# Performance work log

Measured on AMD Instinct MI355X. Metric: run time of the kernel, lower is better.

The kernel has to match this reference:

```python
import jax, jax.numpy as jnp
import numpy as np

E_PHI = 1024
E_F = 1024
HID = 1024
N_HEADS = 16
HEAD_DIM = HID // N_HEADS


def setup_inputs() -> dict:
    key = jax.random.key(0)
    ks = jax.random.split(key, 9)
    B, S = 2, 2048
    s = 0.02
    return {
        "q": jax.random.normal(ks[0], (B, S, E_PHI), jnp.float32),
        "k": jax.random.normal(ks[1], (B, S, E_PHI), jnp.float32),
        "v": jax.random.normal(ks[2], (B, S, E_F), jnp.float32),
        "W_q": jax.random.normal(ks[3], (E_PHI, HID), jnp.float32) * s,
        "W_k": jax.random.normal(ks[4], (E_PHI, HID), jnp.float32) * s,
        "W_v": jax.random.normal(ks[5], (E_F, HID), jnp.float32) * s,
        "b_v": jax.random.normal(ks[6], (HID,), jnp.float32) * s,
        "W_o": jax.random.normal(ks[7], (HID, E_F), jnp.float32) * s,
        "b_o": jax.random.normal(ks[8], (E_F,), jnp.float32) * s,
    }


def reference(q, k, v, W_q, W_k, W_v, b_v, W_o, b_o):
    B, S, _ = q.shape
    # projections -> [B, S, n_heads, head_dim]
    qh = (q @ W_q).reshape(B, S, N_HEADS, HEAD_DIM)
    kh = (k @ W_k).reshape(B, S, N_HEADS, HEAD_DIM)
    vh = (v @ W_v + b_v).reshape(B, S, N_HEADS, HEAD_DIM)

    scale = 1.0 / jnp.sqrt(jnp.float32(HEAD_DIM))
    # scores: [B, H, S_q, S_k]
    scores = jnp.einsum("bihd,bjhd->bhij", qh, kh) * scale

    i = jnp.arange(S)[:, None]
    j = jnp.arange(S)[None, :]
    # strict causal (j < i) plus the single (0,0) entry
    keep = (j < i) | ((i == 0) & (j == 0))
    scores = jnp.where(keep, scores, jnp.float32(-jnp.inf))

    probs = jax.nn.softmax(scores, axis=-1)
    attn = jnp.einsum("bhij,bjhd->bihd", probs, vh).reshape(B, S, HID)
    # dropout is identity in eval mode
    return attn @ W_o + b_o
```

## Files before the change

### kernel.cpp

```cpp
#include <hip/hip_runtime.h>
#include <hip/hip_bf16.h>

typedef __attribute__((ext_vector_type(8))) short bf16x8;
typedef __attribute__((ext_vector_type(4))) float f32x4;
typedef __attribute__((ext_vector_type(4))) unsigned u32x4;

typedef __attribute__((address_space(1))) const void gv_t;
typedef __attribute__((address_space(3))) void lv_t;

static __device__ __forceinline__ void gload16(const void* g, void* l) {
    __builtin_amdgcn_global_load_lds((gv_t*)g, (lv_t*)l, 16, 0, 0);
}

static __device__ __forceinline__ f32x4 mfma16(bf16x8 a, bf16x8 b, f32x4 c) {
    return __builtin_amdgcn_mfma_f32_16x16x32_bf16(a, b, c, 0, 0, 0);
}

static __device__ __forceinline__ unsigned short f2bf(float x) {
    __bf16 b = (__bf16)x;
    return __builtin_bit_cast(unsigned short, b);
}
static __device__ __forceinline__ unsigned pk2(float lo, float hi) {
    return (unsigned)f2bf(lo) | ((unsigned)f2bf(hi) << 16);
}

#define NN 1024
#define KK 1024
#define BK 32
#define NKT (KK / BK)
#define AP 72
#define SOFF2 17.3123404907f

__global__ void cvt3_k(const float* __restrict__ q, const float* __restrict__ k,
                       const float* __restrict__ v, unsigned short* __restrict__ dst)
{
    const int z = blockIdx.y;
    const float* src = (z == 0) ? q : (z == 1) ? k : v;
    unsigned short* d = dst + (size_t)z * 4194304u;
    const size_t i = ((size_t)blockIdx.x * 256 + threadIdx.x) * 8;
    float4 a = *reinterpret_cast<const float4*>(&src[i]);
    float4 b = *reinterpret_cast<const float4*>(&src[i + 4]);
    bf16x8 o;
    o[0] = (short)f2bf(a.x); o[1] = (short)f2bf(a.y);
    o[2] = (short)f2bf(a.z); o[3] = (short)f2bf(a.w);
    o[4] = (short)f2bf(b.x); o[5] = (short)f2bf(b.y);
    o[6] = (short)f2bf(b.z); o[7] = (short)f2bf(b.w);
    *reinterpret_cast<bf16x8*>(&d[i]) = o;
}

__global__ void trcvt_k(const float* __restrict__ w0, const float* __restrict__ w1,
                        const float* __restrict__ w2, const float* __restrict__ w3,
                        unsigned short* __restrict__ dst)
{
    const int z = blockIdx.z;
    const float* W = (z == 0) ? w0 : (z == 1) ? w1 : (z == 2) ? w2 : w3;
    unsigned short* D = dst + (size_t)z * 1048576u;
    __shared__ float t[32][33];
    const int tx = threadIdx.x, ty = threadIdx.y;
    const int x  = blockIdx.x * 32 + tx;
    const int y0 = blockIdx.y * 32;
    for (int i = ty; i < 32; i += 8) t[i][tx] = W[(size_t)(y0 + i) * 1024 + x];
    __syncthreads();
    const int xo = y0 + tx;
    for (int i = ty; i < 32; i += 8)
        D[(size_t)(blockIdx.x * 32 + i) * 1024 + xo] = f2bf(t[tx][i]);
}

__global__ void vtr_k(const unsigned short* __restrict__ vh, unsigned short* __restrict__ vt)
{
    __shared__ unsigned short t[32][33];
    const int bh = blockIdx.z;
    const int b = bh >> 4, h = bh & 15;
    const int s0 = blockIdx.x * 32;
    const int d0 = blockIdx.y * 32;
    const int tx = threadIdx.x, ty = threadIdx.y;
    for (int i = ty; i < 32; i += 8)
        t[i][tx] = vh[(size_t)(b * 2048 + s0 + i) * 1024 + h * 64 + d0 + tx];
    __syncthreads();
    for (int i = ty; i < 32; i += 8)
        vt[((size_t)bh * 64 + d0 + i) * 2048 + s0 + tx] = t[tx][i];
}

template<int MODE>
__global__ __launch_bounds__(256, 2)
void gemm2_k(const unsigned short* __restrict__ Abase,
             const unsigned short* __restrict__ Btbase,
             void* __restrict__ Cbase,
             const float* __restrict__ bias)
{
    __shared__ unsigned short As[2][4096];
    __shared__ unsigned short Bs[2][4096];

    const int f   = blockIdx.x;
    const int xcd = f & 7;
    const int g   = f >> 3;
    const int z   = g >> 5;
    const int rr  = g & 31;
    const int bx  = xcd * 4 + (rr & 3);
    const int by  = rr >> 2;

    const unsigned short* A  = Abase  + (size_t)z * 4194304u;
    const unsigned short* Bt = Btbase + (size_t)z * 1048576u;

    const int tid = threadIdx.x;
    const int wid = tid >> 6, lane = tid & 63;
    const int lg = lane >> 4, lc = lane & 15;
    const int brow = bx * 128;
    const int bcol = by * 128;
    const int wr = (wid >> 1) * 64;
    const int wc = (wid & 1) * 64;

    const int srow = tid >> 2;
    const int scol = (tid & 3) * 8;

    f32x4 acc[4][4];
#pragma unroll
    for (int i = 0; i < 4; ++i)
#pragma unroll
        for (int j = 0; j < 4; ++j) acc[i][j] = (f32x4){0.f, 0.f, 0.f, 0.f};

    gload16(&A [(size_t)(brow + srow)      * KK + scol], &As[0][tid * 8]);
    gload16(&A [(size_t)(brow + 64 + srow) * KK + scol], &As[0][2048 + tid * 8]);
    gload16(&Bt[(size_t)(bcol + srow)      * KK + scol], &Bs[0][tid * 8]);
    gload16(&Bt[(size_t)(bcol + 64 + srow) * KK + scol], &Bs[0][2048 + tid * 8]);
    __syncthreads();

    int cur = 0;
    for (int kt = 0; kt < NKT; ++kt) {
        if (kt + 1 < NKT) {
            const int k0 = (kt + 1) * BK;
            gload16(&A [(size_t)(brow + srow)      * KK + k0 + scol], &As[cur ^ 1][tid * 8]);
            gload16(&A [(size_t)(brow + 64 + srow) * KK + k0 + scol], &As[cur ^ 1][2048 + tid * 8]);
            gload16(&Bt[(size_t)(bcol + srow)      * KK + k0 + scol], &Bs[cur ^ 1][tid * 8]);
            gload16(&Bt[(size_t)(bcol + 64 + srow) * KK + k0 + scol], &Bs[cur ^ 1][2048 + tid * 8]);
        }
        bf16x8 af[4], bfr[4];
#pragma unroll
        for (int i = 0; i < 4; ++i)
            af[i] = *reinterpret_cast<const bf16x8*>(&As[cur][(wr + i * 16 + lc) * 32 + lg * 8]);
#pragma unroll
        for (int j = 0; j < 4; ++j)
            bfr[j] = *reinterpret_cast<const bf16x8*>(&Bs[cur][(wc + j * 16 + lc) * 32 + lg * 8]);
#pragma unroll
        for (int i = 0; i < 4; ++i)
#pragma unroll
            for (int j = 0; j < 4; ++j)
                acc[i][j] = mfma16(af[i], bfr[j], acc[i][j]);
        __syncthreads();
        cur ^= 1;
    }

    float scale = 1.0f;
    const float* bp = nullptr;
    if (MODE == 0) { if (z == 0) scale = 0.18033688f; if (z == 2) bp = bias; }
    else           { bp = bias; }

#pragma unroll
    for (int j = 0; j < 4; ++j) {
        const int col = bcol + wc + j * 16 + lc;
        const float bb = bp ? bp[col] : 0.0f;
#pragma unroll
        for (int i = 0; i < 4; ++i) {
            const int row0 = brow + wr + i * 16 + lg * 4;
#pragma unroll
            for (int r = 0; r < 4; ++r) {
                const float val = acc[i][j][r] * scale + bb;
                if (MODE == 0)
                    ((unsigned short*)Cbase)[(size_t)z * 4194304u + (size_t)(row0 + r) * NN + col] = f2bf(val);
                else
                    ((float*)Cbase)[(size_t)(row0 + r) * NN + col] = val;
            }
        }
    }
}

__global__ __launch_bounds__(256, 4)
void attn_k(const unsigned short* __restrict__ qh,
            const unsigned short* __restrict__ kh,
            const unsigned short* __restrict__ vt,
            unsigned short* __restrict__ out)
{
    __shared__ unsigned short Ks[64 * AP];
    __shared__ unsigned short Vs[64 * AP];

    const int id = blockIdx.x;
    const int u  = id >> 5;
    const int qt = (u < 16) ? u : 47 - u;
    const int bh = (id & 7) * 4 + ((id >> 3) & 3);
    const int b = bh >> 4, h = bh & 15;
    const int tid = threadIdx.x, wid = tid >> 6, lane = tid & 63;
    const int lg = lane >> 4, lc = lane & 15;
    const int q0w = qt * 64 + wid * 16;
    const int hi = lg >> 1;
    const int srcA = ((lg & 1) << 5) | lc;
    const int srcB = srcA + 16;

    const size_t base = (size_t)b * 2048u * 1024u + (size_t)h * 64u;
    const unsigned short* Qb  = qh + base;
    const unsigned short* Kb  = kh + base;
    const unsigned short* Vtb = vt + (size_t)bh * 131072u;

    const int r0 = tid >> 3, kof = (tid & 7) * 8;

    bf16x8 qf[2];
#pragma unroll
    for (int s = 0; s < 2; ++s)
        qf[s] = *reinterpret_cast<const bf16x8*>(&Qb[(size_t)(q0w + lc) * 1024 + s * 32 + lg * 8]);

    f32x4 accT[4];
#pragma unroll
    for (int d = 0; d < 4; ++d) accT[d] = (f32x4){0.f, 0.f, 0.f, 0.f};
    float lsum = 0.f;

    bf16x8 ka0 = *reinterpret_cast<const bf16x8*>(&Kb [(size_t)(r0)      * 1024 + kof]);
    bf16x8 ka1 = *reinterpret_cast<const bf16x8*>(&Kb [(size_t)(32 + r0) * 1024 + kof]);
    bf16x8 va0 = *reinterpret_cast<const bf16x8*>(&Vtb[(size_t)(r0)      * 2048 + kof]);
    bf16x8 va1 = *reinterpret_cast<const bf16x8*>(&Vtb[(size_t)(32 + r0) * 2048 + kof]);

    for (int kt = 0; kt <= qt; ++kt) {
        const int k0 = kt * 64;
        __syncthreads();
        *reinterpret_cast<bf16x8*>(&Ks[(r0)      * AP + kof]) = ka0;
        *reinterpret_cast<bf16x8*>(&Ks[(32 + r0) * AP + kof]) = ka1;
        *reinterpret_cast<bf16x8*>(&Vs[(r0)      * AP + kof]) = va0;
        *reinterpret_cast<bf16x8*>(&Vs[(32 + r0) * AP + kof]) = va1;
        __syncthreads();

        if (kt < qt) {
            const int kn = k0 + 64;
            ka0 = *reinterpret_cast<const bf16x8*>(&Kb [(size_t)(kn + r0)      * 1024 + kof]);
            ka1 = *reinterpret_cast<const bf16x8*>(&Kb [(size_t)(kn + 32 + r0) * 1024 + kof]);
            va0 = *reinterpret_cast<const bf16x8*>(&Vtb[(size_t)(r0)      * 2048 + kn + kof]);
            va1 = *reinterpret_cast<const bf16x8*>(&Vtb[(size_t)(32 + r0) * 2048 + kn + kof]);
        }

        f32x4 sc[4];
#pragma unroll
        for (int g = 0; g < 4; ++g) sc[g] = (f32x4){0.f, 0.f, 0.f, 0.f};
#pragma unroll
        for (int s = 0; s < 2; ++s)
#pragma unroll
            for (int g = 0; g < 4; ++g) {
                bf16x8 kf = *reinterpret_cast<const bf16x8*>(
                    &Ks[(g * 16 + lc) * AP + s * 32 + lg * 8]);
                sc[g] = mfma16(kf, qf[s], sc[g]);
            }

        if (kt == qt) {
            const int qi = q0w + lc;
#pragma unroll
            for (int g = 0; g < 4; ++g)
#pragma unroll
                for (int r = 0; r < 4; ++r) {
                    const int ki = k0 + g * 16 + lg * 4 + r;
                    const bool keep = (ki < qi) || (qi == 0 && ki == 0);
                    if (!keep) sc[g][r] = -1e30f;
                }
        }

        float p[4][4];
#pragma unroll
        for (int g = 0; g < 4; ++g)
#pragma unroll
            for (int r = 0; r < 4; ++r) {
                p[g][r] = exp2f(sc[g][r] - SOFF2);
                lsum += p[g][r];
            }

        unsigned w[4][2];
#pragma unroll
        for (int g = 0; g < 4; ++g) {
            w[g][0] = pk2(p[g][0], p[g][1]);
            w[g][1] = pk2(p[g][2], p[g][3]);
        }

#pragma unroll
        for (int s = 0; s < 2; ++s) {
            unsigned a0A = __shfl(w[2 * s][0],     srcA);
            unsigned a1A = __shfl(w[2 * s][1],     srcA);
            unsigned b0A = __shfl(w[2 * s][0],     srcB);
            unsigned b1A = __shfl(w[2 * s][1],     srcB);
            unsigned a0B = __shfl(w[2 * s + 1][0], srcA);
            unsigned a1B = __shfl(w[2 * s + 1][1], srcA);
            unsigned b0B = __shfl(w[2 * s + 1][0], srcB);
            unsigned b1B = __shfl(w[2 * s + 1][1], srcB);
            u32x4 fr;
            fr[0] = hi ? a0B : a0A;
            fr[1] = hi ? a1B : a1A;
            fr[2] = hi ? b0B : b0A;
            fr[3] = hi ? b1B : b1A;
            bf16x8 pb = __builtin_bit_cast(bf16x8, fr);
#pragma unroll
            for (int di = 0; di < 4; ++di) {
                bf16x8 vf = *reinterpret_cast<const bf16x8*>(
                    &Vs[(di * 16 + lc) * AP + s * 32 + lg * 8]);
                accT[di] = mfma16(vf, pb, accT[di]);
            }
        }
    }

    lsum += __shfl_xor(lsum, 16);
    lsum += __shfl_xor(lsum, 32);
    const float inv = 1.0f / lsum;

    const size_t orow = (size_t)(b * 2048 + q0w + lc) * 1024 + (size_t)h * 64 + lg * 4;
#pragma unroll
    for (int di = 0; di < 4; ++di) {
        unsigned lo  = pk2(accT[di][0] * inv, accT[di][1] * inv);
        unsigned hi2 = pk2(accT[di][2] * inv, accT[di][3] * inv);
        uint2 st; st.x = lo; st.y = hi2;
        *reinterpret_cast<uint2*>(&out[orow + di * 16]) = st;
    }
}

extern "C" void kernel_launch(void* const* d_in, const int* in_sizes, int n_in,
                              void* d_out, int out_size, void* d_ws, size_t ws_size,
                              hipStream_t stream)
{
    const float* q   = (const float*)d_in[0];
    const float* k   = (const float*)d_in[1];
    const float* v   = (const float*)d_in[2];
    const float* W_q = (const float*)d_in[3];
    const float* W_k = (const float*)d_in[4];
    const float* W_v = (const float*)d_in[5];
    const float* b_v = (const float*)d_in[6];
    const float* W_o = (const float*)d_in[7];
    const float* b_o = (const float*)d_in[8];

    char* w = (char*)d_ws;
    unsigned short* qkvb = (unsigned short*)w;
    unsigned short* Wt   = (unsigned short*)(w + 25165824);
    unsigned short* ph   = (unsigned short*)(w + 33554432);
    unsigned short* attn = (unsigned short*)(w + 58720256);
    unsigned short* vt   = qkvb;

    cvt3_k <<<dim3(2048, 3, 1), 256, 0, stream>>>(q, k, v, qkvb);
    trcvt_k<<<dim3(32, 32, 4), dim3(32, 8, 1), 0, stream>>>(W_q, W_k, W_v, W_o, Wt);
    gemm2_k<0><<<dim3(768, 1, 1), 256, 0, stream>>>(qkvb, Wt, ph, b_v);
    vtr_k  <<<dim3(64, 2, 32), dim3(32, 8, 1), 0, stream>>>(ph + 2 * 4194304, vt);
    attn_k <<<dim3(1024, 1, 1), 256, 0, stream>>>(ph, ph + 4194304, vt, attn);
    gemm2_k<1><<<dim3(256, 1, 1), 256, 0, stream>>>(attn, Wt + 3 * 1048576, d_out, b_o);
}
```

Baseline: 133.7 us.

## Triple-buffer GEMM loads with counted waits; double-buffer attention K/V tiles

The GEMM moves from a double-buffered to a triple-buffered LDS pipeline. It prefetches two tiles ahead, waits on vmcnt(4) and uses one barrier per k-step instead of a trailing __syncthreads, so global loads stay in flight across compute. The attention kernel double-buffers its K/V shared tiles, which cuts the two barriers per iteration to one, and raises wave priority around the MFMA blocks with s_setprio. This costs more LDS (for GEMM, 48KB per block), which could reduce occupancy. Relying on hand-counted vmcnt and dropping a barrier also risks races if the load-count assumptions are wrong.

```diff
diff --git a/kernel.cpp b/kernel.cpp
--- a/kernel.cpp
+++ b/kernel.cpp
@@ -88,8 +88,8 @@
              void* __restrict__ Cbase,
              const float* __restrict__ bias)
 {
-    __shared__ unsigned short As[2][4096];
-    __shared__ unsigned short Bs[2][4096];
+    __shared__ unsigned short As[3][4096];
+    __shared__ unsigned short Bs[3][4096];
 
     const int f   = blockIdx.x;
     const int xcd = f & 7;
@@ -119,36 +119,44 @@
 #pragma unroll
         for (int j = 0; j < 4; ++j) acc[i][j] = (f32x4){0.f, 0.f, 0.f, 0.f};
 
-    gload16(&A [(size_t)(brow + srow)      * KK + scol], &As[0][tid * 8]);
-    gload16(&A [(size_t)(brow + 64 + srow) * KK + scol], &As[0][2048 + tid * 8]);
-    gload16(&Bt[(size_t)(bcol + srow)      * KK + scol], &Bs[0][tid * 8]);
-    gload16(&Bt[(size_t)(bcol + 64 + srow) * KK + scol], &Bs[0][2048 + tid * 8]);
-    __syncthreads();
-
-    int cur = 0;
-    for (int kt = 0; kt < NKT; ++kt) {
-        if (kt + 1 < NKT) {
-            const int k0 = (kt + 1) * BK;
-            gload16(&A [(size_t)(brow + srow)      * KK + k0 + scol], &As[cur ^ 1][tid * 8]);
-            gload16(&A [(size_t)(brow + 64 + srow) * KK + k0 + scol], &As[cur ^ 1][2048 + tid * 8]);
-            gload16(&Bt[(size_t)(bcol + srow)      * KK + k0 + scol], &Bs[cur ^ 1][tid * 8]);
-            gload16(&Bt[(size_t)(bcol + 64 + srow) * KK + k0 + scol], &Bs[cur ^ 1][2048 + tid * 8]);
-        }
+    auto issue_tile = [&](int kt, int c) {
+        const int k0 = kt * BK;
+        gload16(&A [(size_t)(brow + srow)      * KK + k0 + scol], &As[c][tid * 8]);
+        gload16(&A [(size_t)(brow + 64 + srow) * KK + k0 + scol], &As[c][2048 + tid * 8]);
+        gload16(&Bt[(size_t)(bcol + srow)      * KK + k0 + scol], &Bs[c][tid * 8]);
+        gload16(&Bt[(size_t)(bcol + 64 + srow) * KK + k0 + scol], &Bs[c][2048 + tid * 8]);
+    };
+    auto compute_tile = [&](int c) {
         bf16x8 af[4], bfr[4];
 #pragma unroll
         for (int i = 0; i < 4; ++i)
-            af[i] = *reinterpret_cast<const bf16x8*>(&As[cur][(wr + i * 16 + lc) * 32 + lg * 8]);
+            af[i] = *reinterpret_cast<const bf16x8*>(&As[c][(wr + i * 16 + lc) * 32 + lg * 8]);
 #pragma unroll
         for (int j = 0; j < 4; ++j)
-            bfr[j] = *reinterpret_cast<const bf16x8*>(&Bs[cur][(wc + j * 16 + lc) * 32 + lg * 8]);
+            bfr[j] = *reinterpret_cast<const bf16x8*>(&Bs[c][(wc + j * 16 + lc) * 32 + lg * 8]);
 #pragma unroll
         for (int i = 0; i < 4; ++i)
 #pragma unroll
             for (int j = 0; j < 4; ++j)
                 acc[i][j] = mfma16(af[i], bfr[j], acc[i][j]);
-        __syncthreads();
-        cur ^= 1;
+    };
+
+    issue_tile(0, 0);
+    issue_tile(1, 1);
+
+    int c0 = 0, c1 = 1, c2 = 2;
+    for (int kt = 0; kt < NKT - 1; ++kt) {
+        asm volatile("s_waitcnt vmcnt(4)" ::: "memory");
+        __builtin_amdgcn_s_barrier();
+        __builtin_amdgcn_sched_barrier(0);
+        if (kt + 2 < NKT) issue_tile(kt + 2, c2);
+        compute_tile(c0);
+        const int t = c0; c0 = c1; c1 = c2; c2 = t;
     }
+    asm volatile("s_waitcnt vmcnt(0)" ::: "memory");
+    __builtin_amdgcn_s_barrier();
+    __builtin_amdgcn_sched_barrier(0);
+    compute_tile(c0);
 
     float scale = 1.0f;
     const float* bp = nullptr;
@@ -180,8 +188,8 @@
             const unsigned short* __restrict__ vt,
             unsigned short* __restrict__ out)
 {
-    __shared__ unsigned short Ks[64 * AP];
-    __shared__ unsigned short Vs[64 * AP];
+    __shared__ unsigned short Ks[2][64 * AP];
+    __shared__ unsigned short Vs[2][64 * AP];
 
     const int id = blockIdx.x;
     const int u  = id >> 5;
@@ -218,13 +226,16 @@
     bf16x8 va1 = *reinterpret_cast<const bf16x8*>(&Vtb[(size_t)(32 + r0) * 2048 + kof]);
 
     for (int kt = 0; kt <= qt; ++kt) {
+        const int cur = kt & 1;
         const int k0 = kt * 64;
-        __syncthreads();
-        *reinterpret_cast<bf16x8*>(&Ks[(r0)      * AP + kof]) = ka0;
-        *reinterpret_cast<bf16x8*>(&Ks[(32 + r0) * AP + kof]) = ka1;
-        *reinterpret_cast<bf16x8*>(&Vs[(r0)      * AP + kof]) = va0;
-        *reinterpret_cast<bf16x8*>(&Vs[(32 + r0) * AP + kof]) = va1;
-        __syncthreads();
+
+        *reinterpret_cast<bf16x8*>(&Ks[cur][(r0)      * AP + kof]) = ka0;
+        *reinterpret_cast<bf16x8*>(&Ks[cur][(32 + r0) * AP + kof]) = ka1;
+        *reinterpret_cast<bf16x8*>(&Vs[cur][(r0)      * AP + kof]) = va0;
+        *reinterpret_cast<bf16x8*>(&Vs[cur][(32 + r0) * AP + kof]) = va1;
+        asm volatile("s_waitcnt lgkmcnt(0)" ::: "memory");
+        __builtin_amdgcn_s_barrier();
+        __builtin_amdgcn_sched_barrier(0);
 
         if (kt < qt) {
             const int kn = k0 + 64;
@@ -237,14 +248,16 @@
         f32x4 sc[4];
 #pragma unroll
         for (int g = 0; g < 4; ++g) sc[g] = (f32x4){0.f, 0.f, 0.f, 0.f};
+        __builtin_amdgcn_s_setprio(1);
 #pragma unroll
         for (int s = 0; s < 2; ++s)
 #pragma unroll
             for (int g = 0; g < 4; ++g) {
                 bf16x8 kf = *reinterpret_cast<const bf16x8*>(
-                    &Ks[(g * 16 + lc) * AP + s * 32 + lg * 8]);
+                    &Ks[cur][(g * 16 + lc) * AP + s * 32 + lg * 8]);
                 sc[g] = mfma16(kf, qf[s], sc[g]);
             }
+        __builtin_amdgcn_s_setprio(0);
 
         if (kt == qt) {
             const int qi = q0w + lc;
@@ -290,12 +303,14 @@
             fr[2] = hi ? b0B : b0A;
             fr[3] = hi ? b1B : b1A;
             bf16x8 pb = __builtin_bit_cast(bf16x8, fr);
+            __builtin_amdgcn_s_setprio(1);
 #pragma unroll
             for (int di = 0; di < 4; ++di) {
                 bf16x8 vf = *reinterpret_cast<const bf16x8*>(
-                    &Vs[(di * 16 + lc) * AP + s * 32 + lg * 8]);
+                    &Vs[cur][(di * 16 + lc) * AP + s * 32 + lg * 8]);
                 accT[di] = mfma16(vf, pb, accT[di]);
             }
+            __builtin_amdgcn_s_setprio(0);
         }
     }
 
```

Result: faster. 126.5 us (-5.4%).
